# Kernel tuning notes

Measured on AMD Instinct MI355X. Metric: run time of the kernel, lower is better.

The kernel has to match this reference:

```python
import jax, jax.numpy as jnp
import numpy as np

B, T, E, C, I_E, O = 4, 2048, 8, 512, 512, 4096


def setup_inputs() -> dict:
    key = jax.random.key(0)
    k1, k2, k3, k4 = jax.random.split(key, 4)
    x = jax.random.normal(k1, (B, E, C, I_E), dtype=jnp.float32)
    combine_array = jax.random.uniform(k2, (B, T, E, C), dtype=jnp.float32)
    W = jax.random.normal(k3, (E, O, I_E), dtype=jnp.float32) * (1.0 / np.sqrt(I_E))
    b = jax.random.normal(k4, (O,), dtype=jnp.float32) * 0.02
    return {"x": x, "combine_array": combine_array, "W": W, "b": b}


def reference(x, combine_array, W, b):
    # per-expert grouped GEMM: [B,E,C,I_e] x [E,O,I_e] -> [B,E,C,O]
    expert_outputs = jnp.einsum('beci,eoi->beco', x, W) + b
    # expert-choice combine: [B,E,C,O] x [B,T,E,C] -> [B,T,O]
    combined = jnp.einsum('beco,btec->bto', expert_outputs, combine_array)
    return combined
```

## Files before the change

### kernel.cpp

```cpp
#include <hip/hip_runtime.h>
#include <hip/hip_bf16.h>
#include <cstdint>

constexpr int NB = 4;
constexpr int NT = 2048;
constexpr int NE = 8;
constexpr int NC = 512;
constexpr int NI = 512;
constexpr int NO = 4096;
constexpr int NEC = NE * NC;

typedef __attribute__((ext_vector_type(8))) short short8;
typedef __attribute__((ext_vector_type(8))) unsigned short ushort8;
typedef __attribute__((ext_vector_type(4))) float f32x4;

__device__ __forceinline__ unsigned short f2bf(float f) {
  unsigned int u = __builtin_bit_cast(unsigned int, f);
  u += 0x7FFFu + ((u >> 16) & 1u);
  return (unsigned short)(u >> 16);
}

__device__ __forceinline__ ushort8 cvt8(float4 a, float4 b) {
  ushort8 v;
  v[0] = f2bf(a.x); v[1] = f2bf(a.y); v[2] = f2bf(a.z); v[3] = f2bf(a.w);
  v[4] = f2bf(b.x); v[5] = f2bf(b.y); v[6] = f2bf(b.z); v[7] = f2bf(b.w);
  return v;
}

__device__ __forceinline__ int lds_byte(int row, int kbyte) {
  return (row * 64 + kbyte) ^ ((row & 6) << 3);
}

__device__ __forceinline__ void gload_lds16(const void* g, void* lds) {
  __builtin_amdgcn_global_load_lds(
      (const __attribute__((address_space(1))) unsigned int*)g,
      (__attribute__((address_space(3))) unsigned int*)lds, 16, 0, 0);
}

__global__ __launch_bounds__(256) void k_cvt(
    const float* __restrict__ src, unsigned short* __restrict__ dst, int n8) {
  int i = blockIdx.x * blockDim.x + threadIdx.x;
  const int stride = gridDim.x * blockDim.x;
  for (; i < n8; i += stride) {
    const float4* s = (const float4*)(src + (size_t)i * 8);
    float4 a = s[0], b = s[1];
    *(ushort8*)(dst + (size_t)i * 8) = cvt8(a, b);
  }
}

template <int NKT>
__device__ __forceinline__ void gemm8_core(
    const unsigned short* __restrict__ Ag,
    const unsigned short* __restrict__ Bg,
    const int ldk, unsigned short* lds, f32x4 (&acc)[8][4]) {
  const int tid = threadIdx.x, lane = tid & 63, wv = tid >> 6;
  const int wr = wv >> 2, wc = wv & 3;
  const int g16 = lane >> 4;
  const int fr  = lane & 15;
  const int pc  = (g16 ^ ((fr >> 1) & 3)) << 4;

  const int scg = (lane & 3) ^ ((lane >> 3) & 3);
  const size_t srow0 = (size_t)(wv * 16 + (lane >> 2)) * ldk + scg * 8;
  const size_t srowstep = (size_t)128 * ldk;
  const int sdst0 = wv * 512;

#define ASLOT(D, KH) ((D) * 16384 + (KH) * 8192)
#define BSLOT(D, KH) (32768 + (D) * 16384 + (KH) * 8192)
#define STG(PTR, SLOT, KT, KH)                                                \
  {                                                                           \
    const unsigned short* _g = (PTR) + srow0 + (size_t)(KT) * 64 + (KH) * 32; \
    gload_lds16(_g, lds + (SLOT) + sdst0);                                    \
    gload_lds16(_g + srowstep, lds + (SLOT) + 4096 + sdst0);                  \
  }
#define RD8(SLOT, R) \
  (*(const short8*)((const char*)lds + (SLOT) * 2 + (R) * 64 + pc))

  short8 af[4], bf[4];

#define LDA4(D, KH, MH)                                             \
  _Pragma("unroll") for (int m = 0; m < 4; ++m) {                   \
    af[m] = RD8(ASLOT(D, KH), wr * 128 + (MH) * 64 + m * 16 + fr);  \
  }
#define LDB4(D, KH)                                                 \
  _Pragma("unroll") for (int n = 0; n < 4; ++n) {                   \
    bf[n] = RD8(BSLOT(D, KH), wc * 64 + n * 16 + fr);               \
  }
#define MFMAQ(MH)                                                    \
  __builtin_amdgcn_s_setprio(1);                                     \
  _Pragma("unroll") for (int m = 0; m < 4; ++m)                      \
  _Pragma("unroll") for (int n = 0; n < 4; ++n) {                    \
    acc[(MH) * 4 + m][n] = __builtin_amdgcn_mfma_f32_16x16x32_bf16(  \
        af[m], bf[n], acc[(MH) * 4 + m][n], 0, 0, 0);                \
  }                                                                  \
  __builtin_amdgcn_s_setprio(0);
#define WAITK()                                        \
  asm volatile("s_waitcnt lgkmcnt(0)" ::: "memory");   \
  __builtin_amdgcn_sched_barrier(0);
#define VM8() asm volatile("s_waitcnt vmcnt(8)" ::: "memory")
#define BAR() __builtin_amdgcn_s_barrier()

  STG(Ag, ASLOT(0, 0), 0, 0); STG(Bg, BSLOT(0, 0), 0, 0);
  STG(Ag, ASLOT(0, 1), 0, 1); STG(Bg, BSLOT(0, 1), 0, 1);
  STG(Ag, ASLOT(1, 0), 1, 0); STG(Bg, BSLOT(1, 0), 1, 0);
  VM8();
  BAR();

  for (int it = 0; it < NKT / 2; ++it) {
    const int k1 = (2 * it + 1) & (NKT - 1);
    const int k2 = (2 * it + 2) & (NKT - 1);
    const int k3 = (2 * it + 3) & (NKT - 1);
    LDA4(0, 0, 0); LDB4(0, 0); STG(Ag, ASLOT(1, 1), k1, 1);
    BAR(); WAITK(); MFMAQ(0); BAR();
    LDA4(0, 0, 1); STG(Bg, BSLOT(1, 1), k1, 1);
    VM8(); BAR(); WAITK(); MFMAQ(1); BAR();
    LDA4(0, 1, 0); LDB4(0, 1); STG(Ag, ASLOT(0, 0), k2, 0);
    BAR(); WAITK(); MFMAQ(0); BAR();
    LDA4(0, 1, 1); STG(Bg, BSLOT(0, 0), k2, 0);
    VM8(); BAR(); WAITK(); MFMAQ(1); BAR();
    LDA4(1, 0, 0); LDB4(1, 0); STG(Ag, ASLOT(0, 1), k2, 1);
    BAR(); WAITK(); MFMAQ(0); BAR();
    LDA4(1, 0, 1); STG(Bg, BSLOT(0, 1), k2, 1);
    VM8(); BAR(); WAITK(); MFMAQ(1); BAR();
    LDA4(1, 1, 0); LDB4(1, 1); STG(Ag, ASLOT(1, 0), k3, 0);
    BAR(); WAITK(); MFMAQ(0); BAR();
    LDA4(1, 1, 1); STG(Bg, BSLOT(1, 0), k3, 0);
    VM8(); BAR(); WAITK(); MFMAQ(1); BAR();
  }
  asm volatile("s_waitcnt vmcnt(0)" ::: "memory");
#undef ASLOT
#undef BSLOT
#undef STG
#undef RD8
#undef LDA4
#undef LDB4
#undef MFMAQ
#undef WAITK
#undef VM8
#undef BAR
}

__global__ __launch_bounds__(512, 2) void k_gemm1p(
    const unsigned short* __restrict__ Wb, const unsigned short* __restrict__ xb,
    const float* __restrict__ bias, unsigned short* __restrict__ eoT) {
  const int bid = (blockIdx.x & 7) * 128 + (blockIdx.x >> 3);
  const int be = bid >> 5, tile = bid & 31;
  const int b = be >> 3, e = be & 7;
  const int bm = tile >> 1, bn = tile & 1;

  const int tid = threadIdx.x, lane = tid & 63, wv = tid >> 6;
  const int wr = wv >> 2, wc = wv & 3;
  const int g16 = lane >> 4, fr = lane & 15;

  const unsigned short* Ag = Wb + (size_t)e * NO * NI + (size_t)(bm * 256) * NI;
  const unsigned short* Bg = xb + ((size_t)b * NE + e) * NC * NI + (size_t)(bn * 256) * NI;

  __shared__ __align__(16) unsigned short lds[65536];

  f32x4 acc[8][4];
#pragma unroll
  for (int m = 0; m < 8; ++m)
#pragma unroll
    for (int n = 0; n < 4; ++n) acc[m][n] = (f32x4)0.f;

  gemm8_core<NI / 64>(Ag, Bg, NI, lds, acc);

  const int o0 = bm * 256 + wr * 128;
  const int c0 = bn * 256 + wc * 64;
#pragma unroll
  for (int i = 0; i < 8; ++i) {
#pragma unroll
    for (int j = 0; j < 4; ++j) {
      const int o = o0 + (i >> 2) * 64 + (i & 3) * 16 + g16 * 4 + j;
      const float bv = bias[o];
      const size_t base = (((size_t)b * NO + o) * NE + e) * NC + c0;
#pragma unroll
      for (int n = 0; n < 4; ++n)
        eoT[base + n * 16 + fr] = f2bf(acc[i][n][j] + bv);
    }
  }
}

__global__ __launch_bounds__(512, 2) void k_gemm2p(
    const unsigned short* __restrict__ cb, const unsigned short* __restrict__ eoT,
    float* __restrict__ out) {
  const int bid = (blockIdx.x & 7) * 64 + (blockIdx.x >> 3);
  const int b  = bid >> 7;
  const int bm = (bid >> 4) & 7;
  const int bn = bid & 15;

  const int tid = threadIdx.x, lane = tid & 63, wv = tid >> 6;
  const int wr = wv >> 2, wc = wv & 3;
  const int g16 = lane >> 4, fr = lane & 15;

  const unsigned short* Ag = cb  + (size_t)b * NT * NEC + (size_t)(bm * 256) * NEC;
  const unsigned short* Bg = eoT + (size_t)b * NO * NEC + (size_t)(bn * 256) * NEC;

  __shared__ __align__(16) unsigned short lds[65536];

  f32x4 acc[8][4];
#pragma unroll
  for (int m = 0; m < 8; ++m)
#pragma unroll
    for (int n = 0; n < 4; ++n) acc[m][n] = (f32x4)0.f;

  gemm8_core<NEC / 64>(Ag, Bg, NEC, lds, acc);

  const int t0 = bm * 256 + wr * 128;
  const int o0 = bn * 256 + wc * 64;
#pragma unroll
  for (int i = 0; i < 8; ++i) {
#pragma unroll
    for (int j = 0; j < 4; ++j) {
      const int t = t0 + (i >> 2) * 64 + (i & 3) * 16 + g16 * 4 + j;
      float* op = out + ((size_t)b * NT + t) * NO + o0;
#pragma unroll
      for (int n = 0; n < 4; ++n) op[n * 16 + fr] = acc[i][n][j];
    }
  }
}

__global__ __launch_bounds__(256, 2) void k_gemm1(
    const float* __restrict__ x, const float* __restrict__ W,
    const float* __restrict__ bias, unsigned short* __restrict__ eoT) {
  const int tile = blockIdx.x;
  const int e = blockIdx.y, b = blockIdx.z;
  const int bm = tile >> 2, bn = tile & 3;
  const int tid = threadIdx.x, lane = tid & 63, wv = tid >> 6;
  const int wr = wv >> 1, wc = wv & 1;

  const float* Ag = W + (size_t)e * NO * NI + (size_t)(bm * 128) * NI;
  const float* Bg = x + ((size_t)b * NE + e) * NC * NI + (size_t)(bn * 128) * NI;

  __shared__ __align__(16) unsigned short As[128 * 32];
  __shared__ __align__(16) unsigned short Bs[128 * 32];

  f32x4 acc[4][4];
#pragma unroll
  for (int m = 0; m < 4; ++m)
#pragma unroll
    for (int n = 0; n < 4; ++n) acc[m][n] = (f32x4)0.f;

  for (int k0 = 0; k0 < NI; k0 += 32) {
    __syncthreads();
#pragma unroll
    for (int s = 0; s < 2; ++s) {
      const int q = tid + s * 256;
      const int row = q >> 2, kc = (q & 3) * 8;
      const float* ga = Ag + (size_t)row * NI + k0 + kc;
      float4 a0 = *(const float4*)ga;
      float4 a1 = *(const float4*)(ga + 4);
      *(ushort8*)((char*)As + lds_byte(row, kc * 2)) = cvt8(a0, a1);
      const float* gb = Bg + (size_t)row * NI + k0 + kc;
      float4 b0 = *(const float4*)gb;
      float4 b1 = *(const float4*)(gb + 4);
      *(ushort8*)((char*)Bs + lds_byte(row, kc * 2)) = cvt8(b0, b1);
    }
    __syncthreads();

    const int kb = (lane >> 4) * 16;
    short8 af[4], bfv[4];
#pragma unroll
    for (int m = 0; m < 4; ++m) {
      const int r = wr * 64 + m * 16 + (lane & 15);
      af[m] = *(const short8*)((const char*)As + lds_byte(r, kb));
    }
#pragma unroll
    for (int n = 0; n < 4; ++n) {
      const int r = wc * 64 + n * 16 + (lane & 15);
      bfv[n] = *(const short8*)((const char*)Bs + lds_byte(r, kb));
    }
#pragma unroll
    for (int m = 0; m < 4; ++m)
#pragma unroll
      for (int n = 0; n < 4; ++n)
        acc[m][n] = __builtin_amdgcn_mfma_f32_16x16x32_bf16(
            af[m], bfv[n], acc[m][n], 0, 0, 0);
  }

  const int o0 = bm * 128 + wr * 64;
  const int c0 = bn * 128 + wc * 64;
#pragma unroll
  for (int m = 0; m < 4; ++m) {
#pragma unroll
    for (int j = 0; j < 4; ++j) {
      const int o = o0 + m * 16 + (lane >> 4) * 4 + j;
      const float bv = bias[o];
      const size_t base = (((size_t)b * NO + o) * NE + e) * NC + c0;
#pragma unroll
      for (int n = 0; n < 4; ++n)
        eoT[base + n * 16 + (lane & 15)] = f2bf(acc[m][n][j] + bv);
    }
  }
}

__global__ __launch_bounds__(256, 2) void k_gemm2(
    const float* __restrict__ comb, const unsigned short* __restrict__ eoT,
    float* __restrict__ out) {
  const int b = blockIdx.y;
  const int bm = blockIdx.x >> 5;
  const int bn = blockIdx.x & 31;
  const int tid = threadIdx.x, lane = tid & 63, wv = tid >> 6;
  const int wr = wv >> 1, wc = wv & 1;

  const float* Ag = comb + (size_t)b * NT * NEC + (size_t)(bm * 128) * NEC;
  const unsigned short* Bg = eoT + (size_t)b * NO * NEC + (size_t)(bn * 128) * NEC;

  __shared__ __align__(16) unsigned short As[128 * 32];
  __shared__ __align__(16) unsigned short Bs[128 * 32];

  f32x4 acc[4][4];
#pragma unroll
  for (int m = 0; m < 4; ++m)
#pragma unroll
    for (int n = 0; n < 4; ++n) acc[m][n] = (f32x4)0.f;

  for (int k0 = 0; k0 < NEC; k0 += 32) {
    __syncthreads();
#pragma unroll
    for (int s = 0; s < 2; ++s) {
      const int q = tid + s * 256;
      const int row = q >> 2, kc = (q & 3) * 8;
      const float* ga = Ag + (size_t)row * NEC + k0 + kc;
      float4 a0 = *(const float4*)ga;
      float4 a1 = *(const float4*)(ga + 4);
      *(ushort8*)((char*)As + lds_byte(row, kc * 2)) = cvt8(a0, a1);
      ushort8 bv = *(const ushort8*)(Bg + (size_t)row * NEC + k0 + kc);
      *(ushort8*)((char*)Bs + lds_byte(row, kc * 2)) = bv;
    }
    __syncthreads();

    const int kb = (lane >> 4) * 16;
    short8 af[4], bfv[4];
#pragma unroll
    for (int m = 0; m < 4; ++m) {
      const int r = wr * 64 + m * 16 + (lane & 15);
      af[m] = *(const short8*)((const char*)As + lds_byte(r, kb));
    }
#pragma unroll
    for (int n = 0; n < 4; ++n) {
      const int r = wc * 64 + n * 16 + (lane & 15);
      bfv[n] = *(const short8*)((const char*)Bs + lds_byte(r, kb));
    }
#pragma unroll
    for (int m = 0; m < 4; ++m)
#pragma unroll
      for (int n = 0; n < 4; ++n)
        acc[m][n] = __builtin_amdgcn_mfma_f32_16x16x32_bf16(
            af[m], bfv[n], acc[m][n], 0, 0, 0);
  }

  const int t0 = bm * 128 + wr * 64;
  const int o0 = bn * 128 + wc * 64;
#pragma unroll
  for (int m = 0; m < 4; ++m) {
#pragma unroll
    for (int j = 0; j < 4; ++j) {
      const int t = t0 + m * 16 + (lane >> 4) * 4 + j;
      float* op = out + ((size_t)b * NT + t) * NO + o0;
#pragma unroll
      for (int n = 0; n < 4; ++n) op[n * 16 + (lane & 15)] = acc[m][n][j];
    }
  }
}

extern "C" void kernel_launch(void* const* d_in, const int* in_sizes, int n_in,
                              void* d_out, int out_size, void* d_ws, size_t ws_size,
                              hipStream_t stream) {
  const float* x    = (const float*)d_in[0];
  const float* comb = (const float*)d_in[1];
  const float* W    = (const float*)d_in[2];
  const float* bias = (const float*)d_in[3];
  float* out = (float*)d_out;

  const size_t EOT_ELEMS = (size_t)NB * NO * NE * NC;
  const size_t X_ELEMS   = (size_t)NB * NE * NC * NI;
  const size_t W_ELEMS   = (size_t)NE * NO * NI;
  const size_t C_ELEMS   = (size_t)NB * NT * NE * NC;
  const size_t region2_elems = (C_ELEMS > X_ELEMS + W_ELEMS) ? C_ELEMS : (X_ELEMS + W_ELEMS);
  const size_t need = (EOT_ELEMS + region2_elems) * 2;

  unsigned short* eoT = (unsigned short*)d_ws;

  if (ws_size >= need) {
    unsigned short* reg2 = eoT + EOT_ELEMS;
    unsigned short* xb = reg2;
    unsigned short* Wb = reg2 + X_ELEMS;
    unsigned short* cbp = reg2;

    k_cvt<<<2048, 256, 0, stream>>>(x, xb, (int)(X_ELEMS / 8));
    k_cvt<<<2048, 256, 0, stream>>>(W, Wb, (int)(W_ELEMS / 8));
    k_gemm1p<<<1024, 512, 0, stream>>>(Wb, xb, bias, eoT);
    k_cvt<<<2048, 256, 0, stream>>>(comb, cbp, (int)(C_ELEMS / 8));
    k_gemm2p<<<512, 512, 0, stream>>>(cbp, eoT, out);
  } else {
    k_gemm1<<<dim3(128, NE, NB), 256, 0, stream>>>(x, W, bias, eoT);
    k_gemm2<<<dim3(512, NB), 256, 0, stream>>>(comb, eoT, out);
  }
}
```

Measured before the change: 403.7 us.

## Double-buffer MFMA fragment registers to overlap LDS reads with matrix math

Splits the A/B fragment registers into two ping-pong sets so LDS reads for the next quarter-step are issued before the MFMAs of the current one. Partial lgkmcnt waits replace full waits, and two of the barriers per sub-step are removed. The aim is to hide LDS read latency behind MFMA execution and to cut barrier stalls. In exchange it uses more VGPRs under launch_bounds(512,2) and depends on fine-grained waitcnt ordering staying correct, so there is some risk of races or register spills.

```diff
diff --git a/kernel.cpp b/kernel.cpp
--- a/kernel.cpp
+++ b/kernel.cpp
@@ -75,58 +75,90 @@
 #define RD8(SLOT, R) \
   (*(const short8*)((const char*)lds + (SLOT) * 2 + (R) * 64 + pc))
 
-  short8 af[4], bf[4];
-
-#define LDA4(D, KH, MH)                                             \
+  short8 afA[4], afB[4], bfA[4], bfB[4];
+
+#define LDA4(SET, D, KH, MH)                                        \
   _Pragma("unroll") for (int m = 0; m < 4; ++m) {                   \
-    af[m] = RD8(ASLOT(D, KH), wr * 128 + (MH) * 64 + m * 16 + fr);  \
-  }
-#define LDB4(D, KH)                                                 \
+    SET[m] = RD8(ASLOT(D, KH), wr * 128 + (MH) * 64 + m * 16 + fr); \
+  }
+#define LDB4(SET, D, KH)                                            \
   _Pragma("unroll") for (int n = 0; n < 4; ++n) {                   \
-    bf[n] = RD8(BSLOT(D, KH), wc * 64 + n * 16 + fr);               \
-  }
-#define MFMAQ(MH)                                                    \
+    SET[n] = RD8(BSLOT(D, KH), wc * 64 + n * 16 + fr);              \
+  }
+#define MFMAQ(ASET, BSET, MH)                                        \
   __builtin_amdgcn_s_setprio(1);                                     \
   _Pragma("unroll") for (int m = 0; m < 4; ++m)                      \
   _Pragma("unroll") for (int n = 0; n < 4; ++n) {                    \
     acc[(MH) * 4 + m][n] = __builtin_amdgcn_mfma_f32_16x16x32_bf16(  \
-        af[m], bf[n], acc[(MH) * 4 + m][n], 0, 0, 0);                \
+        ASET[m], BSET[n], acc[(MH) * 4 + m][n], 0, 0, 0);            \
   }                                                                  \
   __builtin_amdgcn_s_setprio(0);
-#define WAITK()                                        \
-  asm volatile("s_waitcnt lgkmcnt(0)" ::: "memory");   \
-  __builtin_amdgcn_sched_barrier(0);
-#define VM8() asm volatile("s_waitcnt vmcnt(8)" ::: "memory")
+#define LG4()                                          \
+  asm volatile("s_waitcnt lgkmcnt(4)" ::: "memory");   \
+  __builtin_amdgcn_sched_barrier(0)
+#define LG8()                                          \
+  asm volatile("s_waitcnt lgkmcnt(8)" ::: "memory");   \
+  __builtin_amdgcn_sched_barrier(0)
+#define VM6() asm volatile("s_waitcnt vmcnt(6)" ::: "memory")
 #define BAR() __builtin_amdgcn_s_barrier()
 
   STG(Ag, ASLOT(0, 0), 0, 0); STG(Bg, BSLOT(0, 0), 0, 0);
   STG(Ag, ASLOT(0, 1), 0, 1); STG(Bg, BSLOT(0, 1), 0, 1);
   STG(Ag, ASLOT(1, 0), 1, 0); STG(Bg, BSLOT(1, 0), 1, 0);
-  VM8();
+  asm volatile("s_waitcnt vmcnt(8)" ::: "memory");
   BAR();
+  LDA4(afA, 0, 0, 0); LDB4(bfA, 0, 0);
 
   for (int it = 0; it < NKT / 2; ++it) {
     const int k1 = (2 * it + 1) & (NKT - 1);
     const int k2 = (2 * it + 2) & (NKT - 1);
     const int k3 = (2 * it + 3) & (NKT - 1);
-    LDA4(0, 0, 0); LDB4(0, 0); STG(Ag, ASLOT(1, 1), k1, 1);
-    BAR(); WAITK(); MFMAQ(0); BAR();
-    LDA4(0, 0, 1); STG(Bg, BSLOT(1, 1), k1, 1);
-    VM8(); BAR(); WAITK(); MFMAQ(1); BAR();
-    LDA4(0, 1, 0); LDB4(0, 1); STG(Ag, ASLOT(0, 0), k2, 0);
-    BAR(); WAITK(); MFMAQ(0); BAR();
-    LDA4(0, 1, 1); STG(Bg, BSLOT(0, 0), k2, 0);
-    VM8(); BAR(); WAITK(); MFMAQ(1); BAR();
-    LDA4(1, 0, 0); LDB4(1, 0); STG(Ag, ASLOT(0, 1), k2, 1);
-    BAR(); WAITK(); MFMAQ(0); BAR();
-    LDA4(1, 0, 1); STG(Bg, BSLOT(0, 1), k2, 1);
-    VM8(); BAR(); WAITK(); MFMAQ(1); BAR();
-    LDA4(1, 1, 0); LDB4(1, 1); STG(Ag, ASLOT(1, 0), k3, 0);
-    BAR(); WAITK(); MFMAQ(0); BAR();
-    LDA4(1, 1, 1); STG(Bg, BSLOT(1, 0), k3, 0);
-    VM8(); BAR(); WAITK(); MFMAQ(1); BAR();
-  }
-  asm volatile("s_waitcnt vmcnt(0)" ::: "memory");
+    STG(Ag, ASLOT(1, 1), k1, 1);
+    VM6();
+    LDA4(afB, 0, 0, 1);
+    LG4();
+    MFMAQ(afA, bfA, 0);
+    BAR();
+    STG(Bg, BSLOT(1, 1), k1, 1);
+    LDA4(afA, 0, 1, 0); LDB4(bfB, 0, 1);
+    LG8();
+    MFMAQ(afB, bfA, 1);
+    BAR();
+    STG(Ag, ASLOT(0, 0), k2, 0);
+    VM6();
+    LDA4(afB, 0, 1, 1);
+    LG4();
+    MFMAQ(afA, bfB, 0);
+    BAR();
+    STG(Bg, BSLOT(0, 0), k2, 0);
+    LDA4(afA, 1, 0, 0); LDB4(bfA, 1, 0);
+    LG8();
+    MFMAQ(afB, bfB, 1);
+    BAR();
+    STG(Ag, ASLOT(0, 1), k2, 1);
+    VM6();
+    LDA4(afB, 1, 0, 1);
+    LG4();
+    MFMAQ(afA, bfA, 0);
+    BAR();
+    STG(Bg, BSLOT(0, 1), k2, 1);
+    LDA4(afA, 1, 1, 0); LDB4(bfB, 1, 1);
+    LG8();
+    MFMAQ(afB, bfA, 1);
+    BAR();
+    STG(Ag, ASLOT(1, 0), k3, 0);
+    VM6();
+    LDA4(afB, 1, 1, 1);
+    LG4();
+    MFMAQ(afA, bfB, 0);
+    BAR();
+    STG(Bg, BSLOT(1, 0), k3, 0);
+    LDA4(afA, 0, 0, 0); LDB4(bfA, 0, 0);
+    LG8();
+    MFMAQ(afB, bfB, 1);
+    BAR();
+  }
+  asm volatile("s_waitcnt vmcnt(0) lgkmcnt(0)" ::: "memory");
 #undef ASLOT
 #undef BSLOT
 #undef STG
@@ -134,8 +166,9 @@
 #undef LDA4
 #undef LDB4
 #undef MFMAQ
-#undef WAITK
-#undef VM8
+#undef LG4
+#undef LG8
+#undef VM6
 #undef BAR
 }
 
```

Measured after the change: 396.6 us. No clear change (-1.8%).
